# Kernel tuning notes

Hardware: AMD Instinct MI355X
Metric: run time of the kernel (lower is better)

## Reference

```python
import jax, jax.numpy as jnp
import numpy as np


def _squash(t):
    # squash along axis=2 (the atoms axis of [B, D, A, 1, 1])
    norm = jnp.linalg.norm(t, axis=2, keepdims=True)
    n2 = norm * norm
    return t / norm * (n2 / (1.0 + n2))


def setup_inputs() -> dict:
    key = jax.random.key(0)
    k1, k2 = jax.random.split(key)
    B, I, Ain, D, A = 32, 2048, 16, 32, 16
    x = jax.random.normal(k1, (B, I, Ain, 1, 1), jnp.float32)
    weights = 0.1 * jax.random.normal(k2, (I, Ain, D * A, 1, 1), jnp.float32)
    bias = jnp.full((D, A, 1, 1), 0.1, jnp.float32)  # nn.init.constant_(0.1)
    return {"x": x, "weights": weights, "bias": bias, "num_routing": 3}


def reference(x, weights, bias, num_routing):
    B, I, Ain = x.shape[:3]
    D, A = bias.shape[:2]
    # Vote computation (standard voting): sum over input_atoms.
    # Torch does expand+mul+sum; einsum is the same math without the 4.8GB intermediate.
    votes = jnp.einsum('bia,iao->bio', x[:, :, :, 0, 0],
                       weights[:, :, :, 0, 0]).reshape(B, I, D, A, 1, 1)
    votes_sg = jax.lax.stop_gradient(votes)  # votes_trans_stopped in torch
    logits = jnp.zeros((B, I, D, 1, 1), x.dtype)
    activation = None
    for i in range(num_routing):
        route = jax.nn.softmax(logits, axis=2)  # [B, I, D, 1, 1], softmax over D
        v = votes if i == num_routing - 1 else votes_sg
        # route broadcast over atoms axis; sum over input capsules I
        preact = jnp.sum(route[:, :, :, None] * v, axis=1) + bias  # [B, D, A, 1, 1]
        activation = _squash(preact)
        if i < num_routing - 1:
            # agreement update uses non-stopped votes (as in torch)
            logits = logits + jnp.sum(votes * activation[:, None], axis=3)  # [B, I, D, 1, 1]
    return activation
```

## Files before the change

### kernel.cpp

```cpp
#include <hip/hip_runtime.h>


#define B_  32
#define I_  2048
#define K_  16
#define O_  512
#define NG_ 256
#define IC_ 8

template<int PASS>
__global__ __launch_bounds__(256)
void sweep_kernel(const float* __restrict__ x, const float* __restrict__ W,
                  const float* __restrict__ act0_g, const float* __restrict__ act1_g,
                  float* __restrict__ partial)
{
    const int tid  = threadIdx.x;
    const int lane = tid & 63;
    const int wave = tid >> 6;
    const int ig   = blockIdx.x >> 1;
    const int bh   = blockIdx.x & 1;
    const int d    = lane & 31;
    const int h    = lane >> 5;
    const int obase = d * 16 + h * 8;

    __shared__ float sW[K_ * O_];
    __shared__ float sX[16 * K_];

    float facc[4][8];
    #pragma unroll
    for (int bb = 0; bb < 4; ++bb)
        #pragma unroll
        for (int j = 0; j < 8; ++j) facc[bb][j] = 0.f;

    float a0[4][8], a1[4][8];
    if (PASS >= 1) {
        #pragma unroll
        for (int bb = 0; bb < 4; ++bb) {
            const int b = bh * 16 + wave * 4 + bb;
            const float4* p = (const float4*)(act0_g + b * O_ + obase);
            float4 f0 = p[0], f1 = p[1];
            a0[bb][0]=f0.x; a0[bb][1]=f0.y; a0[bb][2]=f0.z; a0[bb][3]=f0.w;
            a0[bb][4]=f1.x; a0[bb][5]=f1.y; a0[bb][6]=f1.z; a0[bb][7]=f1.w;
        }
    }
    if (PASS == 2) {
        #pragma unroll
        for (int bb = 0; bb < 4; ++bb) {
            const int b = bh * 16 + wave * 4 + bb;
            const float4* p = (const float4*)(act1_g + b * O_ + obase);
            float4 f0 = p[0], f1 = p[1];
            a1[bb][0]=f0.x; a1[bb][1]=f0.y; a1[bb][2]=f0.z; a1[bb][3]=f0.w;
            a1[bb][4]=f1.x; a1[bb][5]=f1.y; a1[bb][6]=f1.z; a1[bb][7]=f1.w;
        }
    }

    for (int ii = 0; ii < IC_; ++ii) {
        const int i = ig * IC_ + ii;
        __syncthreads();
        {
            const float4* Wg = (const float4*)(W + (size_t)i * (K_ * O_));
            #pragma unroll
            for (int q = 0; q < 8; ++q) {
                const int f = tid + 256 * q;
                float4 w4 = Wg[f];
                const int flat = 4 * f;
                const int k  = flat >> 9;
                const int o  = flat & (O_ - 1);
                const int dd = o >> 4;
                const int aa = o & 15;
                const int hh = aa >> 3;
                const int j0 = aa & 7;
                const int base = k * O_ + hh * 32 + dd;
                sW[base + (j0 + 0) * 64] = w4.x;
                sW[base + (j0 + 1) * 64] = w4.y;
                sW[base + (j0 + 2) * 64] = w4.z;
                sW[base + (j0 + 3) * 64] = w4.w;
            }
        }
        sX[tid & 255] = x[((size_t)(bh * 16 + (tid >> 4)) * I_ + i) * K_ + (tid & 15)];
        __syncthreads();

        float V[4][8];
        #pragma unroll
        for (int bb = 0; bb < 4; ++bb)
            #pragma unroll
            for (int j = 0; j < 8; ++j) V[bb][j] = 0.f;
        #pragma unroll
        for (int k = 0; k < K_; ++k) {
            float w[8];
            #pragma unroll
            for (int j = 0; j < 8; ++j) w[j] = sW[k * O_ + j * 64 + lane];
            #pragma unroll
            for (int bb = 0; bb < 4; ++bb) {
                const float xb = sX[(wave * 4 + bb) * K_ + k];
                #pragma unroll
                for (int j = 0; j < 8; ++j) V[bb][j] = fmaf(xb, w[j], V[bb][j]);
            }
        }

        #pragma unroll
        for (int bb = 0; bb < 4; ++bb) {
            if (PASS == 0) {
                #pragma unroll
                for (int j = 0; j < 8; ++j) facc[bb][j] += V[bb][j];
            } else {
                float p0 = 0.f;
                #pragma unroll
                for (int j = 0; j < 8; ++j) p0 = fmaf(V[bb][j], a0[bb][j], p0);
                p0 += __shfl_xor(p0, 32);
                float lg = p0;
                if (PASS == 2) {
                    float p1 = 0.f;
                    #pragma unroll
                    for (int j = 0; j < 8; ++j) p1 = fmaf(V[bb][j], a1[bb][j], p1);
                    p1 += __shfl_xor(p1, 32);
                    lg += p1;
                }
                float mx = lg;
                mx = fmaxf(mx, __shfl_xor(mx, 1));
                mx = fmaxf(mx, __shfl_xor(mx, 2));
                mx = fmaxf(mx, __shfl_xor(mx, 4));
                mx = fmaxf(mx, __shfl_xor(mx, 8));
                mx = fmaxf(mx, __shfl_xor(mx, 16));
                const float e = __expf(lg - mx);
                float s = e;
                s += __shfl_xor(s, 1);
                s += __shfl_xor(s, 2);
                s += __shfl_xor(s, 4);
                s += __shfl_xor(s, 8);
                s += __shfl_xor(s, 16);
                const float r = e * __builtin_amdgcn_rcpf(s);
                #pragma unroll
                for (int j = 0; j < 8; ++j)
                    facc[bb][j] = fmaf(r, V[bb][j], facc[bb][j]);
            }
        }
    }

    #pragma unroll
    for (int bb = 0; bb < 4; ++bb) {
        const int b = bh * 16 + wave * 4 + bb;
        float4* dst = (float4*)(partial + ((size_t)ig * B_ + b) * O_ + obase);
        dst[0] = make_float4(facc[bb][0], facc[bb][1], facc[bb][2], facc[bb][3]);
        dst[1] = make_float4(facc[bb][4], facc[bb][5], facc[bb][6], facc[bb][7]);
    }
}

__global__ __launch_bounds__(256)
void reduce_squash(const float* __restrict__ partial, const float* __restrict__ bias,
                   float scale, float* __restrict__ out)
{
    const int t  = threadIdx.x;
    const int g  = blockIdx.x * 64 + (t & 63);
    const int ws = t >> 6;
    float s = 0.f;
    #pragma unroll 8
    for (int w = ws * 64; w < ws * 64 + 64; ++w)
        s += partial[(size_t)w * (B_ * O_) + g];
    __shared__ float red[256];
    red[t] = s;
    __syncthreads();
    if (t < 64) {
        s = red[t] + red[t + 64] + red[t + 128] + red[t + 192];
        const float p = fmaf(s, scale, bias[g & (O_ - 1)]);
        float nn = p * p;
        nn += __shfl_xor(nn, 1);
        nn += __shfl_xor(nn, 2);
        nn += __shfl_xor(nn, 4);
        nn += __shfl_xor(nn, 8);
        out[g] = p * sqrtf(nn) / (1.f + nn);
    }
}

extern "C" void kernel_launch(void* const* d_in, const int* in_sizes, int n_in,
                              void* d_out, int out_size, void* d_ws, size_t ws_size,
                              hipStream_t stream) {
    const float* x    = (const float*)d_in[0];
    const float* W    = (const float*)d_in[1];
    const float* bias = (const float*)d_in[2];
    float* out = (float*)d_out;

    float* partial = (float*)d_ws;
    float* act0    = partial + (size_t)NG_ * B_ * O_;
    float* act1    = act0 + B_ * O_;

    sweep_kernel<0><<<NG_ * 2, 256, 0, stream>>>(x, W, nullptr, nullptr, partial);
    reduce_squash<<<256, 256, 0, stream>>>(partial, bias, 1.f / 32.f, act0);
    sweep_kernel<1><<<NG_ * 2, 256, 0, stream>>>(x, W, act0, nullptr, partial);
    reduce_squash<<<256, 256, 0, stream>>>(partial, bias, 1.f, act1);
    sweep_kernel<2><<<NG_ * 2, 256, 0, stream>>>(x, W, act0, act1, partial);
    reduce_squash<<<256, 256, 0, stream>>>(partial, bias, 1.f, out);
}
```

Measured before the change: 225.5 us.

## Relayout shared weights for float4 reads, register x, drop softmax max

Lanes are remapped so each d-pair sits in adjacent lanes. Shared weights are stored so each lane reads two float4 vectors per k, replacing eight scalar LDS reads. The x tile is loaded straight into registers from global memory instead of through shared memory. The softmax max-subtraction is removed, which risks overflow if logits grow large. The reduce kernel is retuned to 512 blocks with 8 slices of 32, giving more parallelism in the partial-sum reduction.

Result: faster. 188.4 us (-16.4%).

```diff
diff --git a/kernel.cpp b/kernel.cpp
--- a/kernel.cpp
+++ b/kernel.cpp
@@ -19,12 +19,14 @@
     const int wave = tid >> 6;
     const int ig   = blockIdx.x >> 1;
     const int bh   = blockIdx.x & 1;
-    const int d    = lane & 31;
-    const int h    = lane >> 5;
+    const int d    = lane >> 1;
+    const int h    = lane & 1;
     const int obase = d * 16 + h * 8;
 
+    const int wv   = __builtin_amdgcn_readfirstlane(wave);
+    const int bbase = bh * 16 + wv * 4;
+
     __shared__ float sW[K_ * O_];
-    __shared__ float sX[16 * K_];
 
     float facc[4][8];
     #pragma unroll
@@ -36,8 +38,7 @@
     if (PASS >= 1) {
         #pragma unroll
         for (int bb = 0; bb < 4; ++bb) {
-            const int b = bh * 16 + wave * 4 + bb;
-            const float4* p = (const float4*)(act0_g + b * O_ + obase);
+            const float4* p = (const float4*)(act0_g + (bbase + bb) * O_ + obase);
             float4 f0 = p[0], f1 = p[1];
             a0[bb][0]=f0.x; a0[bb][1]=f0.y; a0[bb][2]=f0.z; a0[bb][3]=f0.w;
             a0[bb][4]=f1.x; a0[bb][5]=f1.y; a0[bb][6]=f1.z; a0[bb][7]=f1.w;
@@ -46,8 +47,7 @@
     if (PASS == 2) {
         #pragma unroll
         for (int bb = 0; bb < 4; ++bb) {
-            const int b = bh * 16 + wave * 4 + bb;
-            const float4* p = (const float4*)(act1_g + b * O_ + obase);
+            const float4* p = (const float4*)(act1_g + (bbase + bb) * O_ + obase);
             float4 f0 = p[0], f1 = p[1];
             a1[bb][0]=f0.x; a1[bb][1]=f0.y; a1[bb][2]=f0.z; a1[bb][3]=f0.w;
             a1[bb][4]=f1.x; a1[bb][5]=f1.y; a1[bb][6]=f1.z; a1[bb][7]=f1.w;
@@ -61,23 +61,28 @@
             const float4* Wg = (const float4*)(W + (size_t)i * (K_ * O_));
             #pragma unroll
             for (int q = 0; q < 8; ++q) {
-                const int f = tid + 256 * q;
+                const int f  = tid + 256 * q;
                 float4 w4 = Wg[f];
-                const int flat = 4 * f;
-                const int k  = flat >> 9;
-                const int o  = flat & (O_ - 1);
+                const int e0 = 4 * f;
+                const int k  = e0 >> 9;
+                const int o  = e0 & (O_ - 1);
                 const int dd = o >> 4;
                 const int aa = o & 15;
                 const int hh = aa >> 3;
-                const int j0 = aa & 7;
-                const int base = k * O_ + hh * 32 + dd;
-                sW[base + (j0 + 0) * 64] = w4.x;
-                sW[base + (j0 + 1) * 64] = w4.y;
-                sW[base + (j0 + 2) * 64] = w4.z;
-                sW[base + (j0 + 3) * 64] = w4.w;
+                const int jq = (aa >> 2) & 1;
+                *(float4*)&sW[jq * 4096 + k * 256 + (dd * 2 + hh) * 4] = w4;
             }
         }
-        sX[tid & 255] = x[((size_t)(bh * 16 + (tid >> 4)) * I_ + i) * K_ + (tid & 15)];
+        float xs[4][16];
+        #pragma unroll
+        for (int bb = 0; bb < 4; ++bb) {
+            const float4* xp = (const float4*)(x + ((size_t)(bbase + bb) * I_ + i) * K_);
+            #pragma unroll
+            for (int q = 0; q < 4; ++q) {
+                float4 v = xp[q];
+                xs[bb][4*q+0]=v.x; xs[bb][4*q+1]=v.y; xs[bb][4*q+2]=v.z; xs[bb][4*q+3]=v.w;
+            }
+        }
         __syncthreads();
 
         float V[4][8];
@@ -87,12 +92,12 @@
             for (int j = 0; j < 8; ++j) V[bb][j] = 0.f;
         #pragma unroll
         for (int k = 0; k < K_; ++k) {
-            float w[8];
-            #pragma unroll
-            for (int j = 0; j < 8; ++j) w[j] = sW[k * O_ + j * 64 + lane];
+            const float4 w0 = *(const float4*)&sW[k * 256 + lane * 4];
+            const float4 w1 = *(const float4*)&sW[4096 + k * 256 + lane * 4];
+            const float w[8] = {w0.x, w0.y, w0.z, w0.w, w1.x, w1.y, w1.z, w1.w};
             #pragma unroll
             for (int bb = 0; bb < 4; ++bb) {
-                const float xb = sX[(wave * 4 + bb) * K_ + k];
+                const float xb = xs[bb][k];
                 #pragma unroll
                 for (int j = 0; j < 8; ++j) V[bb][j] = fmaf(xb, w[j], V[bb][j]);
             }
@@ -107,28 +112,22 @@
                 float p0 = 0.f;
                 #pragma unroll
                 for (int j = 0; j < 8; ++j) p0 = fmaf(V[bb][j], a0[bb][j], p0);
-                p0 += __shfl_xor(p0, 32);
+                p0 += __shfl_xor(p0, 1);
                 float lg = p0;
                 if (PASS == 2) {
                     float p1 = 0.f;
                     #pragma unroll
                     for (int j = 0; j < 8; ++j) p1 = fmaf(V[bb][j], a1[bb][j], p1);
-                    p1 += __shfl_xor(p1, 32);
+                    p1 += __shfl_xor(p1, 1);
                     lg += p1;
                 }
-                float mx = lg;
-                mx = fmaxf(mx, __shfl_xor(mx, 1));
-                mx = fmaxf(mx, __shfl_xor(mx, 2));
-                mx = fmaxf(mx, __shfl_xor(mx, 4));
-                mx = fmaxf(mx, __shfl_xor(mx, 8));
-                mx = fmaxf(mx, __shfl_xor(mx, 16));
-                const float e = __expf(lg - mx);
+                const float e = __expf(lg);
                 float s = e;
-                s += __shfl_xor(s, 1);
                 s += __shfl_xor(s, 2);
                 s += __shfl_xor(s, 4);
                 s += __shfl_xor(s, 8);
                 s += __shfl_xor(s, 16);
+                s += __shfl_xor(s, 32);
                 const float r = e * __builtin_amdgcn_rcpf(s);
                 #pragma unroll
                 for (int j = 0; j < 8; ++j)
@@ -139,7 +138,7 @@
 
     #pragma unroll
     for (int bb = 0; bb < 4; ++bb) {
-        const int b = bh * 16 + wave * 4 + bb;
+        const int b = bbase + bb;
         float4* dst = (float4*)(partial + ((size_t)ig * B_ + b) * O_ + obase);
         dst[0] = make_float4(facc[bb][0], facc[bb][1], facc[bb][2], facc[bb][3]);
         dst[1] = make_float4(facc[bb][4], facc[bb][5], facc[bb][6], facc[bb][7]);
@@ -151,18 +150,20 @@
                    float scale, float* __restrict__ out)
 {
     const int t  = threadIdx.x;
-    const int g  = blockIdx.x * 64 + (t & 63);
-    const int ws = t >> 6;
+    const int g  = blockIdx.x * 32 + (t & 31);
+    const int sl = t >> 5;
     float s = 0.f;
-    #pragma unroll 8
-    for (int w = ws * 64; w < ws * 64 + 64; ++w)
+    #pragma unroll
+    for (int w = sl * 32; w < sl * 32 + 32; ++w)
         s += partial[(size_t)w * (B_ * O_) + g];
     __shared__ float red[256];
     red[t] = s;
     __syncthreads();
-    if (t < 64) {
-        s = red[t] + red[t + 64] + red[t + 128] + red[t + 192];
-        const float p = fmaf(s, scale, bias[g & (O_ - 1)]);
+    if (t < 32) {
+        float v = red[t];
+        #pragma unroll
+        for (int r = 1; r < 8; ++r) v += red[t + 32 * r];
+        const float p = fmaf(v, scale, bias[g & (O_ - 1)]);
         float nn = p * p;
         nn += __shfl_xor(nn, 1);
         nn += __shfl_xor(nn, 2);
@@ -185,9 +186,9 @@
     float* act1    = act0 + B_ * O_;
 
     sweep_kernel<0><<<NG_ * 2, 256, 0, stream>>>(x, W, nullptr, nullptr, partial);
-    reduce_squash<<<256, 256, 0, stream>>>(partial, bias, 1.f / 32.f, act0);
+    reduce_squash<<<512, 256, 0, stream>>>(partial, bias, 1.f / 32.f, act0);
     sweep_kernel<1><<<NG_ * 2, 256, 0, stream>>>(x, W, act0, nullptr, partial);
-    reduce_squash<<<256, 256, 0, stream>>>(partial, bias, 1.f, act1);
+    reduce_squash<<<512, 256, 0, stream>>>(partial, bias, 1.f, act1);
     sweep_kernel<2><<<NG_ * 2, 256, 0, stream>>>(x, W, act0, act1, partial);
-    reduce_squash<<<256, 256, 0, stream>>>(partial, bias, 1.f, out);
+    reduce_squash<<<512, 256, 0, stream>>>(partial, bias, 1.f, out);
 }
```
